# Kernel optimization log

Hardware: AMD Instinct MI355X
Metric: run time of the kernel (lower is better)

Reference implementation:

```python
import jax, jax.numpy as jnp
import numpy as np

N_E = 8192
E_DIM = 64
BETA = 0.25


def setup_inputs() -> dict:
    key = jax.random.key(0)
    k_z, k_e = jax.random.split(key)
    z = jax.random.normal(k_z, (16, E_DIM, 64, 64), dtype=jnp.float32)  # b c h w
    # nn.Embedding weight init: uniform(-1/n_e, 1/n_e)
    embedding = jax.random.uniform(
        k_e, (N_E, E_DIM), dtype=jnp.float32, minval=-1.0 / N_E, maxval=1.0 / N_E
    )
    return {"z": z, "embedding": embedding}


def reference(z, embedding):
    # b c h w -> b h w c
    zc = jnp.transpose(z, (0, 2, 3, 1))
    zf = zc.reshape(-1, embedding.shape[1])  # [N, d]
    # squared euclidean distances: ||z||^2 + ||e||^2 - 2 z.e
    d = (
        jnp.sum(zf * zf, axis=1, keepdims=True)
        + jnp.sum(embedding * embedding, axis=1)
        - 2.0 * jnp.einsum("nd,kd->nk", zf, embedding)
    )  # [N, K]
    min_encoding_indices = jnp.argmin(d, axis=1)  # [N]
    z_q = jnp.take(embedding, min_encoding_indices, axis=0).reshape(zc.shape)
    # legacy=True loss
    loss = jnp.mean((jax.lax.stop_gradient(z_q) - zc) ** 2) + BETA * jnp.mean(
        (z_q - jax.lax.stop_gradient(zc)) ** 2
    )
    # straight-through estimator
    z_q = zc + jax.lax.stop_gradient(z_q - zc)
    z_q = jnp.transpose(z_q, (0, 3, 1, 2))  # b h w c -> b c h w
    return z_q, loss, min_encoding_indices
```

## Files before the change

kernel.cpp:

```cpp
#include <hip/hip_runtime.h>

#define NTOT 65536
#define KC   8192
#define DV   64
#define ZQN  4194304
#define NSPL 4
#define KSL  2048
#define TILE 128
#define NTILE 16
#define CAP2 16
#define SLA  44u
#define SLE  40u

typedef unsigned int u32;
typedef unsigned long long u64;
typedef unsigned short ushort;
typedef short short8 __attribute__((ext_vector_type(8)));
typedef float float4v __attribute__((ext_vector_type(4)));

__device__ __forceinline__ short f2bf(float x) {
    u32 u = __float_as_uint(x);
    u32 r = (u + 0x7fffu + ((u >> 16) & 1u)) >> 16;
    return (short)r;
}

__device__ __forceinline__ float exact_d(float A, float B,
                                         const float* __restrict__ zr,
                                         const float* __restrict__ e) {
#pragma clang fp contract(off)
    float u0 = 0.f, u1 = 0.f, u2 = 0.f, u3 = 0.f;
#pragma unroll
    for (int i = 0; i < 4; ++i) {
        const int t = 16 * i;
        u0 = (zr[t+0]*e[t+0]) + ((zr[t+4]*e[t+4]) + ((zr[t+8]*e[t+8]) + ((zr[t+12]*e[t+12]) + u0)));
        u1 = (zr[t+1]*e[t+1]) + ((zr[t+5]*e[t+5]) + ((zr[t+9]*e[t+9]) + ((zr[t+13]*e[t+13]) + u1)));
        u2 = (zr[t+2]*e[t+2]) + ((zr[t+6]*e[t+6]) + ((zr[t+10]*e[t+10]) + ((zr[t+14]*e[t+14]) + u2)));
        u3 = (zr[t+3]*e[t+3]) + ((zr[t+7]*e[t+7]) + ((zr[t+11]*e[t+11]) + ((zr[t+15]*e[t+15]) + u3)));
    }
    float dot = (u0 + u1) + (u2 + u3);
    return (A + B) - (2.0f * dot);
}

__global__ __launch_bounds__(256) void vq_prep(
    const float* __restrict__ emb, float* __restrict__ nrm,
    u32* __restrict__ cnt, double* __restrict__ lacc,
    u32* __restrict__ oflowCnt, ushort* __restrict__ ebs) {
    const int tid = blockIdx.x * 256 + threadIdx.x;
    const int t = tid >> 10, r = tid & 1023;
    const int s = r >> 7, r2 = r & 127, h = r2 >> 6, l = r2 & 63;
    const int q = l >> 4, c = l & 15;
    const float* src = emb + (size_t)((t * 128 + s * 16 + c) * 64 + h * 32 + q * 8);
    short8 v;
#pragma unroll
    for (int j = 0; j < 8; ++j) v[j] = f2bf(src[j]);
    *reinterpret_cast<short8*>(ebs + (size_t)tid * 8) = v;
    cnt[tid] = 0u;
    if (tid < KC) {
        double sacc = 0.0;
#pragma unroll
        for (int d = 0; d < DV; ++d) {
            double x = (double)emb[(size_t)tid * DV + d];
            sacc = fma(x, x, sacc);
        }
        nrm[tid] = (float)sacc;
    }
    if (tid == 0) { *lacc = 0.0; *oflowCnt = 0u; }
}

__global__ __launch_bounds__(256, 4) void vq_pass(
    const float* __restrict__ z, const ushort* __restrict__ ebs,
    u32* __restrict__ cnt, u32* __restrict__ cand) {
    __shared__ ushort tileS[TILE * DV];
    const int tid = threadIdx.x;
    const int lane = tid & 63, wv = tid >> 6;
    const int nblk = blockIdx.x & 255, ks = blockIdx.x >> 8;
    const int nb = nblk * 256 + wv * 64;
    const int col = lane & 15, quad = lane >> 4;
    const int nlo = nb + col;

    short8 zf[4][2];
#pragma unroll
    for (int ns = 0; ns < 4; ++ns) {
        int n = nlo + ns * 16;
        const float* zp = z + (size_t)(n >> 12) * 262144 + (n & 4095);
#pragma unroll
        for (int t2 = 0; t2 < 2; ++t2)
#pragma unroll
            for (int j = 0; j < 8; ++j)
                zf[ns][t2][j] = f2bf(zp[(size_t)(t2 * 32 + quad * 8 + j) * 4096]);
    }

    u32 r0[4] = {0, 0, 0, 0}, r1[4] = {0, 0, 0, 0}, r2[4] = {0, 0, 0, 0};
    const char* gs = (const char*)ebs + (size_t)ks * (KSL * DV * 2);

    int4 pre[4];
#pragma unroll
    for (int j = 0; j < 4; ++j)
        pre[j] = *reinterpret_cast<const int4*>(gs + j * 4096 + tid * 16);

    for (int t = 0; t < NTILE; ++t) {
        __syncthreads();
#pragma unroll
        for (int j = 0; j < 4; ++j)
            *reinterpret_cast<int4*>((char*)tileS + j * 4096 + tid * 16) = pre[j];
        __syncthreads();
        if (t < NTILE - 1) {
#pragma unroll
            for (int j = 0; j < 4; ++j)
                pre[j] = *reinterpret_cast<const int4*>(
                    gs + (size_t)(t + 1) * 16384 + j * 4096 + tid * 16);
        }
#pragma unroll
        for (int s = 0; s < 8; ++s) {
            const char* tb = (const char*)tileS + s * 2048;
            short8 a0 = *reinterpret_cast<const short8*>(tb + lane * 16);
            short8 a1 = *reinterpret_cast<const short8*>(tb + 1024 + lane * 16);
            const u32 lowc = 0x80000000u + (u32)((((t << 3) | s) << 2) | quad);
#pragma unroll
            for (int ns = 0; ns < 4; ++ns) {
                float4v acc = {0.f, 0.f, 0.f, 0.f};
                acc = __builtin_amdgcn_mfma_f32_16x16x32_bf16(a0, zf[ns][0], acc, 0, 0, 0);
                acc = __builtin_amdgcn_mfma_f32_16x16x32_bf16(a1, zf[ns][1], acc, 0, 0, 0);
                float m4 = fmaxf(fmaxf(acc[0], acc[1]), fmaxf(acc[2], acc[3]));
                u32 e = ((u32)(int)(m4 * 1048576.0f) << 16) + lowc;
                u32 x  = min(r0[ns], e);
                r0[ns] = max(r0[ns], e);
                u32 y  = min(r1[ns], x);
                r1[ns] = max(r1[ns], x);
                r2[ns] = max(r2[ns], y);
            }
        }
    }

#pragma unroll
    for (int ns = 0; ns < 4; ++ns) {
        u32 m = r0[ns];
        m = max(m, __shfl_xor(m, 16));
        m = max(m, __shfl_xor(m, 32));
        const u32 thr = (m & 0xffff0000u) - (SLA << 16);
        const int n = nlo + ns * 16;
        const u32 tag = (u32)ks << 9;
        if (r0[ns] >= thr) {
            u32 p = atomicAdd(&cnt[n], 1u);
            if (p < CAP2) cand[(size_t)n * CAP2 + p] = r0[ns] | tag;
        }
        if (r1[ns] >= thr) {
            u32 p = atomicAdd(&cnt[n], 1u);
            if (p < CAP2) cand[(size_t)n * CAP2 + p] = r1[ns] | tag;
        }
        if (r2[ns] >= thr) {
            u32 p = atomicAdd(&cnt[n], 1u);
            if (p < CAP2) cand[(size_t)n * CAP2 + p] = r2[ns] | tag;
        }
    }
}

__global__ __launch_bounds__(256) void vq_e1(
    const float* __restrict__ z, const float* __restrict__ emb,
    const float* __restrict__ nrm, const u32* __restrict__ cnt,
    const u32* __restrict__ cand, int* __restrict__ idxw,
    float* __restrict__ out, u32* __restrict__ oflowCnt,
    int* __restrict__ oflowList) {
    const int n = blockIdx.x * 256 + threadIdx.x;
    u32 c = cnt[n];
    if (c > CAP2) {
        u32 p = atomicAdd(oflowCnt, 1u);
        oflowList[p] = n;
        idxw[n] = 0;
        out[(size_t)ZQN + 1 + n] = 0.f;
        return;
    }
    u32 emax = 0u;
    for (u32 j = 0; j < c; ++j) {
        u32 e = cand[(size_t)n * CAP2 + j];
        if (e > emax) emax = e;
    }
    const u32 ethr = (emax & 0xffff0000u) - (SLE << 16);

    const float* zp = z + (size_t)(n >> 12) * 262144 + (n & 4095);
    float zr[DV];
#pragma unroll
    for (int d = 0; d < DV; ++d) zr[d] = zp[(size_t)d * 4096];
    double ad = 0.0;
#pragma unroll
    for (int d = 0; d < DV; ++d) ad = fma((double)zr[d], (double)zr[d], ad);
    const float A = (float)ad;

    float dmin = 1e30f;
    int kmin = 0x7fffffff;
    for (u32 j = 0; j < c; ++j) {
        u32 e = cand[(size_t)n * CAP2 + j];
        if (e < ethr) continue;
        int s    = (int)(e >> 9) & 3;
        int step = (int)(e >> 2) & 127;
        int q    = (int)e & 3;
        int base = s * KSL + step * 16 + q * 4;
#pragma unroll
        for (int r = 0; r < 4; ++r) {
            int k = base + r;
            float d = exact_d(A, nrm[k], zr, emb + (size_t)k * DV);
            if (d < dmin || (d == dmin && k < kmin)) { dmin = d; kmin = k; }
        }
    }
    idxw[n] = kmin;
    out[(size_t)ZQN + 1 + n] = (float)kmin;
}

__global__ __launch_bounds__(256) void vq_e1b(
    const float* __restrict__ z, const float* __restrict__ emb,
    const float* __restrict__ nrm, const u32* __restrict__ oflowCnt,
    const int* __restrict__ oflowList, int* __restrict__ idxw,
    float* __restrict__ out) {
    __shared__ u64 red[4];
    const int tid = threadIdx.x;
    const int nof = (int)*oflowCnt;
    for (int i = blockIdx.x; i < nof; i += gridDim.x) {
        const int n = oflowList[i];
        const float* zp = z + (size_t)(n >> 12) * 262144 + (n & 4095);
        float zr[DV];
#pragma unroll
        for (int d = 0; d < DV; ++d) zr[d] = zp[(size_t)d * 4096];
        double ad = 0.0;
#pragma unroll
        for (int d = 0; d < DV; ++d) ad = fma((double)zr[d], (double)zr[d], ad);
        const float A = (float)ad;
        u64 best = ~0ull;
        for (int k = tid; k < KC; k += 256) {
            float d = exact_d(A, nrm[k], zr, emb + (size_t)k * DV);
            u64 key = ((u64)__float_as_uint(d) << 32) | (u32)k;
            if (key < best) best = key;
        }
#pragma unroll
        for (int off = 32; off > 0; off >>= 1) {
            u64 o = __shfl_down(best, off, 64);
            if (o < best) best = o;
        }
        if ((tid & 63) == 0) red[tid >> 6] = best;
        __syncthreads();
        if (tid == 0) {
            u64 b = red[0];
#pragma unroll
            for (int w = 1; w < 4; ++w) if (red[w] < b) b = red[w];
            int kmin = (int)(b & 0xffffffffu);
            idxw[n] = kmin;
            out[(size_t)ZQN + 1 + n] = (float)kmin;
        }
        __syncthreads();
    }
}

__global__ __launch_bounds__(256) void vq_e2(
    const float* __restrict__ z, const float* __restrict__ emb,
    const int* __restrict__ idxw, float* __restrict__ out,
    double* __restrict__ lacc) {
    __shared__ double red[4];
    const int tid = threadIdx.x;
    const int n = blockIdx.x * 256 + tid;
    const int b = n >> 12, hw = n & 4095;
    const int kmin = idxw[n];
    const float* zp = z + (size_t)b * 262144 + hw;
    const float* erow = emb + (size_t)kmin * DV;
    double lsum = 0.0;
#pragma unroll
    for (int c = 0; c < DV; ++c) {
        float v = erow[c];
        out[(size_t)b * 262144 + (size_t)c * 4096 + hw] = v;
        double dv = (double)v - (double)zp[(size_t)c * 4096];
        lsum = fma(dv, dv, lsum);
    }
#pragma unroll
    for (int off = 32; off > 0; off >>= 1)
        lsum += __shfl_down(lsum, off, 64);
    if ((tid & 63) == 0) red[tid >> 6] = lsum;
    __syncthreads();
    if (tid == 0)
        atomicAdd(lacc, red[0] + red[1] + red[2] + red[3]);
}

__global__ void vq_fin(const double* __restrict__ lacc, float* __restrict__ out) {
    if (threadIdx.x == 0)
        out[ZQN] = (float)(1.25 * (*lacc) / (double)ZQN);
}

extern "C" void kernel_launch(void* const* d_in, const int* in_sizes, int n_in,
                              void* d_out, int out_size, void* d_ws, size_t ws_size,
                              hipStream_t stream) {
    const float* z   = (const float*)d_in[0];
    const float* emb = (const float*)d_in[1];
    float* out = (float*)d_out;

    ushort* ebs  = (ushort*)d_out;
    u32*    cand = (u32*)((char*)d_out + 1048576);
    double* lacc  = (double*)d_ws;
    u32*    oflowCnt = (u32*)((char*)d_ws + 8);
    float*  nrm   = (float*)((char*)d_ws + 64);
    u32*    cnt   = (u32*)((char*)d_ws + 32832);
    int*    idxw  = (int*)((char*)d_ws + 294976);
    int*    oflowList = (int*)((char*)d_ws + 557120);

    vq_prep<<<256, 256, 0, stream>>>(emb, nrm, cnt, lacc, oflowCnt, ebs);
    vq_pass<<<NSPL * 256, 256, 0, stream>>>(z, ebs, cnt, cand);
    vq_e1<<<256, 256, 0, stream>>>(z, emb, nrm, cnt, cand, idxw, out,
                                   oflowCnt, oflowList);
    vq_e1b<<<128, 256, 0, stream>>>(z, emb, nrm, oflowCnt, oflowList, idxw, out);
    vq_e2<<<256, 256, 0, stream>>>(z, emb, idxw, out, lacc);
    vq_fin<<<1, 64, 0, stream>>>(lacc, out);
}
```

Baseline: 251.4 us.

## Coarsen candidate tracking to 32-code groups and parallelize refinement and output kernels

The screening pass now takes the max over two adjacent 16-code MFMA tiles before top-3 insertion. This halves the packing and min/max work per tile but doubles the codes each candidate expands to. The refinement kernel splits each row's candidate list across 4 lanes and reduces with shuffles, and the output kernel splits each row's 64 channels across 4 waves with float4 loads. Both kernels launch 4x more blocks to raise parallelism. Occupancy is now requested with the waves_per_eu attribute instead of the launch_bounds minimum.

```diff
diff --git a/kernel.cpp b/kernel.cpp
--- a/kernel.cpp
+++ b/kernel.cpp
@@ -67,14 +67,14 @@
     if (tid == 0) { *lacc = 0.0; *oflowCnt = 0u; }
 }
 
-__global__ __launch_bounds__(256, 4) void vq_pass(
-    const float* __restrict__ z, const ushort* __restrict__ ebs,
-    u32* __restrict__ cnt, u32* __restrict__ cand) {
+__global__ __launch_bounds__(256) __attribute__((amdgpu_waves_per_eu(4, 4)))
+void vq_pass(const float* __restrict__ z, const ushort* __restrict__ ebs,
+             u32* __restrict__ cnt, u32* __restrict__ cand) {
     __shared__ ushort tileS[TILE * DV];
     const int tid = threadIdx.x;
-    const int lane = tid & 63, wv = tid >> 6;
+    const int lane = tid & 63;
     const int nblk = blockIdx.x & 255, ks = blockIdx.x >> 8;
-    const int nb = nblk * 256 + wv * 64;
+    const int nb = nblk * 256 + (tid >> 6) * 64;
     const int col = lane & 15, quad = lane >> 4;
     const int nlo = nb + col;
 
@@ -111,18 +111,24 @@
                     gs + (size_t)(t + 1) * 16384 + j * 4096 + tid * 16);
         }
 #pragma unroll
-        for (int s = 0; s < 8; ++s) {
-            const char* tb = (const char*)tileS + s * 2048;
-            short8 a0 = *reinterpret_cast<const short8*>(tb + lane * 16);
-            short8 a1 = *reinterpret_cast<const short8*>(tb + 1024 + lane * 16);
-            const u32 lowc = 0x80000000u + (u32)((((t << 3) | s) << 2) | quad);
+        for (int g2 = 0; g2 < 4; ++g2) {
+            const char* tb = (const char*)tileS + g2 * 4096;
+            short8 a00 = *reinterpret_cast<const short8*>(tb + lane * 16);
+            short8 a01 = *reinterpret_cast<const short8*>(tb + 1024 + lane * 16);
+            short8 a10 = *reinterpret_cast<const short8*>(tb + 2048 + lane * 16);
+            short8 a11 = *reinterpret_cast<const short8*>(tb + 3072 + lane * 16);
+            const u32 lowc = 0x80000000u + (u32)(((t * 4 + g2) << 2) | quad);
 #pragma unroll
             for (int ns = 0; ns < 4; ++ns) {
-                float4v acc = {0.f, 0.f, 0.f, 0.f};
-                acc = __builtin_amdgcn_mfma_f32_16x16x32_bf16(a0, zf[ns][0], acc, 0, 0, 0);
-                acc = __builtin_amdgcn_mfma_f32_16x16x32_bf16(a1, zf[ns][1], acc, 0, 0, 0);
-                float m4 = fmaxf(fmaxf(acc[0], acc[1]), fmaxf(acc[2], acc[3]));
-                u32 e = ((u32)(int)(m4 * 1048576.0f) << 16) + lowc;
+                float4v acc0 = {0.f, 0.f, 0.f, 0.f};
+                float4v acc1 = {0.f, 0.f, 0.f, 0.f};
+                acc0 = __builtin_amdgcn_mfma_f32_16x16x32_bf16(a00, zf[ns][0], acc0, 0, 0, 0);
+                acc0 = __builtin_amdgcn_mfma_f32_16x16x32_bf16(a01, zf[ns][1], acc0, 0, 0, 0);
+                acc1 = __builtin_amdgcn_mfma_f32_16x16x32_bf16(a10, zf[ns][0], acc1, 0, 0, 0);
+                acc1 = __builtin_amdgcn_mfma_f32_16x16x32_bf16(a11, zf[ns][1], acc1, 0, 0, 0);
+                float m = fmaxf(fmaxf(fmaxf(acc0[0], acc0[1]), fmaxf(acc0[2], acc0[3])),
+                                fmaxf(fmaxf(acc1[0], acc1[1]), fmaxf(acc1[2], acc1[3])));
+                u32 e = ((u32)(int)(m * 1048576.0f) << 16) + lowc;
                 u32 x  = min(r0[ns], e);
                 r0[ns] = max(r0[ns], e);
                 u32 y  = min(r1[ns], x);
@@ -139,7 +145,7 @@
         m = max(m, __shfl_xor(m, 32));
         const u32 thr = (m & 0xffff0000u) - (SLA << 16);
         const int n = nlo + ns * 16;
-        const u32 tag = (u32)ks << 9;
+        const u32 tag = (u32)ks << 8;
         if (r0[ns] >= thr) {
             u32 p = atomicAdd(&cnt[n], 1u);
             if (p < CAP2) cand[(size_t)n * CAP2 + p] = r0[ns] | tag;
@@ -161,13 +167,16 @@
     const u32* __restrict__ cand, int* __restrict__ idxw,
     float* __restrict__ out, u32* __restrict__ oflowCnt,
     int* __restrict__ oflowList) {
-    const int n = blockIdx.x * 256 + threadIdx.x;
+    const int gid = blockIdx.x * 256 + threadIdx.x;
+    const int n = gid >> 2, j4 = gid & 3;
     u32 c = cnt[n];
     if (c > CAP2) {
-        u32 p = atomicAdd(oflowCnt, 1u);
-        oflowList[p] = n;
-        idxw[n] = 0;
-        out[(size_t)ZQN + 1 + n] = 0.f;
+        if (j4 == 0) {
+            u32 p = atomicAdd(oflowCnt, 1u);
+            oflowList[p] = n;
+            idxw[n] = 0;
+            out[(size_t)ZQN + 1 + n] = 0.f;
+        }
         return;
     }
     u32 emax = 0u;
@@ -188,22 +197,30 @@
 
     float dmin = 1e30f;
     int kmin = 0x7fffffff;
-    for (u32 j = 0; j < c; ++j) {
+    for (u32 j = (u32)j4; j < c; j += 4) {
         u32 e = cand[(size_t)n * CAP2 + j];
         if (e < ethr) continue;
-        int s    = (int)(e >> 9) & 3;
-        int step = (int)(e >> 2) & 127;
-        int q    = (int)e & 3;
-        int base = s * KSL + step * 16 + q * 4;
-#pragma unroll
-        for (int r = 0; r < 4; ++r) {
-            int k = base + r;
-            float d = exact_d(A, nrm[k], zr, emb + (size_t)k * DV);
-            if (d < dmin || (d == dmin && k < kmin)) { dmin = d; kmin = k; }
-        }
-    }
-    idxw[n] = kmin;
-    out[(size_t)ZQN + 1 + n] = (float)kmin;
+        int s   = (int)(e >> 8) & 3;
+        int grp = (int)(e >> 2) & 63;
+        int q   = (int)e & 3;
+        int base = s * KSL + grp * 32 + q * 4;
+#pragma unroll
+        for (int st = 0; st < 2; ++st)
+#pragma unroll
+            for (int r = 0; r < 4; ++r) {
+                int k = base + st * 16 + r;
+                float d = exact_d(A, nrm[k], zr, emb + (size_t)k * DV);
+                if (d < dmin || (d == dmin && k < kmin)) { dmin = d; kmin = k; }
+            }
+    }
+    u64 key = ((u64)__float_as_uint(dmin) << 32) | (u32)kmin;
+    u64 o1 = __shfl_xor(key, 1, 64); if (o1 < key) key = o1;
+    u64 o2 = __shfl_xor(key, 2, 64); if (o2 < key) key = o2;
+    if (j4 == 0) {
+        int km = (int)(key & 0xffffffffu);
+        idxw[n] = km;
+        out[(size_t)ZQN + 1 + n] = (float)km;
+    }
 }
 
 __global__ __launch_bounds__(256) void vq_e1b(
@@ -255,18 +272,24 @@
     double* __restrict__ lacc) {
     __shared__ double red[4];
     const int tid = threadIdx.x;
-    const int n = blockIdx.x * 256 + tid;
+    const int n = blockIdx.x * 64 + (tid & 63);
+    const int part = tid >> 6;
     const int b = n >> 12, hw = n & 4095;
     const int kmin = idxw[n];
     const float* zp = z + (size_t)b * 262144 + hw;
-    const float* erow = emb + (size_t)kmin * DV;
+    const float4* er4 = (const float4*)(emb + (size_t)kmin * DV + part * 16);
     double lsum = 0.0;
 #pragma unroll
-    for (int c = 0; c < DV; ++c) {
-        float v = erow[c];
-        out[(size_t)b * 262144 + (size_t)c * 4096 + hw] = v;
-        double dv = (double)v - (double)zp[(size_t)c * 4096];
-        lsum = fma(dv, dv, lsum);
+    for (int i4 = 0; i4 < 4; ++i4) {
+        float4 ev = er4[i4];
+#pragma unroll
+        for (int u = 0; u < 4; ++u) {
+            int c = part * 16 + i4 * 4 + u;
+            float v = (u == 0) ? ev.x : (u == 1) ? ev.y : (u == 2) ? ev.z : ev.w;
+            out[(size_t)b * 262144 + (size_t)c * 4096 + hw] = v;
+            double dv = (double)v - (double)zp[(size_t)c * 4096];
+            lsum = fma(dv, dv, lsum);
+        }
     }
 #pragma unroll
     for (int off = 32; off > 0; off >>= 1)
@@ -300,9 +323,9 @@
 
     vq_prep<<<256, 256, 0, stream>>>(emb, nrm, cnt, lacc, oflowCnt, ebs);
     vq_pass<<<NSPL * 256, 256, 0, stream>>>(z, ebs, cnt, cand);
-    vq_e1<<<256, 256, 0, stream>>>(z, emb, nrm, cnt, cand, idxw, out,
-                                   oflowCnt, oflowList);
+    vq_e1<<<1024, 256, 0, stream>>>(z, emb, nrm, cnt, cand, idxw, out,
+                                    oflowCnt, oflowList);
     vq_e1b<<<128, 256, 0, stream>>>(z, emb, nrm, oflowCnt, oflowList, idxw, out);
-    vq_e2<<<256, 256, 0, stream>>>(z, emb, idxw, out, lacc);
+    vq_e2<<<1024, 256, 0, stream>>>(z, emb, idxw, out, lacc);
     vq_fin<<<1, 64, 0, stream>>>(lacc, out);
 }
```

New measurement: 245.1 us. 2.5% less time.
